# Kernel optimization log

Measured on AMD Instinct MI355X. Metric: run time of the kernel, lower is better.

The kernel has to match this reference:

```python
import jax, jax.numpy as jnp
import numpy as np

T, B, NIN, N, A = 100, 32, 512, 2048, 2
DT = 1e-3
THR = 1.0
ALPHA = float(np.exp(-DT / 0.01))


def setup_inputs() -> dict:
    key = jax.random.key(0)
    k1, k2, k3, k4 = jax.random.split(key, 4)
    rates = jax.random.uniform(k1, (T, B, NIN), dtype=jnp.float32) * 100.0  # Hz
    noise = jax.random.uniform(k2, (T, B, NIN), dtype=jnp.float32)  # Poisson thresholds
    Win = jax.random.normal(k3, (A, NIN, N), dtype=jnp.float32) * (1.5 / np.sqrt(NIN))
    Wrec = jax.random.normal(k4, (A, A, N, N), dtype=jnp.float32) * (1.0 / np.sqrt(N))
    return {"rates": rates, "noise": noise, "Win": Win, "Wrec": Wrec}


def reference(rates, noise, Win, Wrec):
    dtype = rates.dtype
    V0 = jnp.zeros((A, B, N), dtype)   # membrane potentials, all areas
    Xd0 = jnp.zeros((A, B, N), dtype)  # delayed cross-area spikes (reset())

    def step(carry, inp):
        V, Xd = carry
        rate_t, noise_t = inp
        # PoissonInput: Bernoulli spikes with prob rate*dt
        Xi = (noise_t < rate_t * DT).astype(dtype)  # [B, NIN]
        # per-area input current: feedforward + all-to-all cross-area recurrent
        I = jnp.einsum('bi,ain->abn', Xi, Win) + jnp.einsum('sbn,sanm->abm', Xd, Wrec)
        # LIF: leak, reset on previous spike, integrate
        V_new = ALPHA * V * (1.0 - Xd) + I
        S = (V_new >= THR).astype(dtype)  # [A, B, N]
        return (V_new, S), (Xi, S)

    (_, _), (Xis, Ss) = jax.lax.scan(step, (V0, Xd0), (rates, noise))
    # Xis: [T, B, NIN]; Ss: [T, A, B, N] -> per-area stacked outputs
    return (Xis, Ss[:, 0], Ss[:, 1])
```

## Files before the change

kernel.cpp:

```cpp
#include <hip/hip_runtime.h>

#define T_STEPS 100
#define BATCH   32
#define NIN     512
#define NN      2048
#define AREAS   2

#define ALPHA_D 0.9048374180359595

__global__ __launch_bounds__(256)
void k0_xi(const float* __restrict__ rates, const float* __restrict__ noise,
           float* __restrict__ outXi, unsigned* __restrict__ xi_mask)
{
    int el = blockIdx.x * 256 + threadIdx.x;
    float r = rates[el], nz = noise[el];
    float p = __fmul_rn(r, 0.001f);
    int spike = (nz < p) ? 1 : 0;
    outXi[el] = (float)spike;
    if (spike) {
        int t = el >> 14;
        int b = (el >> 9) & 31;
        int i = el & (NIN - 1);
        atomicOr(&xi_mask[(t * 32 + b) * 16 + (i >> 5)], 1u << (i & 31));
    }
}

__global__ __launch_bounds__(256)
void k_ff(const float* __restrict__ Win, const unsigned* __restrict__ xi_mask,
          float* __restrict__ Iff)
{
    const int tb  = blockIdx.x;
    const int a   = blockIdx.y;
    const int tid = threadIdx.x;

    __shared__ unsigned mws[16];
    if (tid < 16) mws[tid] = xi_mask[tb * 16 + tid];
    __syncthreads();

    const float* Wa = Win + ((size_t)a << 20) + (tid << 3);
    float4 A0 = {0,0,0,0}, A1 = {0,0,0,0};
    for (int w = 0; w < 16; ++w) {
        unsigned mw = mws[w];
        int base_i = w << 5;
        while (mw) {
            int i = base_i + (__ffs(mw) - 1);
            mw &= mw - 1;
            const float* rp = Wa + ((size_t)i << 11);
            float4 w0 = ((const float4*)rp)[0];
            float4 w1 = ((const float4*)rp)[1];
            A0.x += w0.x; A0.y += w0.y; A0.z += w0.z; A0.w += w0.w;
            A1.x += w1.x; A1.y += w1.y; A1.z += w1.z; A1.w += w1.w;
        }
    }
    float* op = Iff + (((size_t)tb * 2 + a) << 11) + (tid << 3);
    ((float4*)op)[0] = A0;
    ((float4*)op)[1] = A1;
}

#define OFF_OF(rr) ((((rr) >> 11) << 23) + (((rr) & 2047) << 11))

__device__ __forceinline__ void issue8(const float* __restrict__ Wa,
                                       const unsigned short* lp, float* p)
{
    uint4 u = *(const uint4*)lp;
    p[0] = Wa[OFF_OF((int)(u.x & 0xffff))];
    p[1] = Wa[OFF_OF((int)(u.x >> 16))];
    p[2] = Wa[OFF_OF((int)(u.y & 0xffff))];
    p[3] = Wa[OFF_OF((int)(u.y >> 16))];
    p[4] = Wa[OFF_OF((int)(u.z & 0xffff))];
    p[5] = Wa[OFF_OF((int)(u.z >> 16))];
    p[6] = Wa[OFF_OF((int)(u.w & 0xffff))];
    p[7] = Wa[OFF_OF((int)(u.w >> 16))];
}

__global__ __launch_bounds__(256, 2)
void k_steps(const float* __restrict__ Wrec,
             unsigned long long* __restrict__ smask,
             const float* __restrict__ Iff,
             float* __restrict__ outS)
{
    const int tid = threadIdx.x;
    const int bx  = blockIdx.x;
    const int s   = bx & 15;
    const int b   = bx >> 4;
    const int a   = s >> 3;
    const int m0  = (s & 7) << 8;
    const int c   = m0 + tid;

    __shared__ unsigned mws[128];
    __shared__ __align__(16) unsigned short lrec[AREAS * NN];
    __shared__ int base[128];
    __shared__ int cnt_rec;
    __shared__ unsigned nsp[8];

    const float* __restrict__ Wa = Wrec + ((size_t)a << 22) + c;
    const int rr_self = (a << 11) | c;
    const int wsel = rr_self >> 5;
    const int w0   = s << 3;

    float vst = 0.0f;

    for (int t = 0; t < T_STEPS; ++t) {
        unsigned long long* cur = smask + (size_t)(t & 1) * (BATCH * 128) + (b << 7);
        unsigned long long* nxt = smask + (size_t)((t + 1) & 1) * (BATCH * 128) + (b << 7);

        if (tid < 128) {
            unsigned long long v = __hip_atomic_load(&cur[tid], __ATOMIC_RELAXED,
                                                     __HIP_MEMORY_SCOPE_AGENT);
            while ((unsigned)(v >> 32) != (unsigned)t) {
                __builtin_amdgcn_s_sleep(4);
                v = __hip_atomic_load(&cur[tid], __ATOMIC_RELAXED,
                                      __HIP_MEMORY_SCOPE_AGENT);
            }
            mws[tid] = (unsigned)v;
        }
        if (tid < 8) nsp[tid] = 0u;
        float accf = Iff[((((size_t)t * BATCH + b) * 2 + a) << 11) + c];
        __syncthreads();

        if (tid < 64) {
            int c0 = __popc(mws[2 * tid]), c1 = __popc(mws[2 * tid + 1]);
            int cc = c0 + c1, incl = cc;
            #pragma unroll
            for (int d = 1; d < 64; d <<= 1) {
                int v = __shfl_up(incl, d, 64);
                if (tid >= d) incl += v;
            }
            base[2 * tid]     = incl - cc;
            base[2 * tid + 1] = incl - c1;
            if (tid == 63) cnt_rec = incl;
        }
        __syncthreads();

        if (tid < 128) {
            unsigned w = mws[tid];
            if (w) {
                int off = base[tid];
                int bb = tid << 5;
                while (w) {
                    int p = __ffs(w) - 1;
                    lrec[off++] = (unsigned short)(bb + p);
                    w &= w - 1;
                }
            }
        }
        __syncthreads();

        const int nrec = cnt_rec;
        unsigned xd = (mws[wsel] >> (tid & 31)) & 1u;

        float accr = 0.0f;
        int j = 0;
        if (nrec >= 32) {
            float p[32], q[32];
            issue8(Wa, &lrec[0],  p + 0);
            issue8(Wa, &lrec[8],  p + 8);
            issue8(Wa, &lrec[16], p + 16);
            issue8(Wa, &lrec[24], p + 24);
            for (j = 32; j + 32 <= nrec; j += 32) {
                issue8(Wa, &lrec[j],      q + 0);
                issue8(Wa, &lrec[j + 8],  q + 8);
                issue8(Wa, &lrec[j + 16], q + 16);
                issue8(Wa, &lrec[j + 24], q + 24);
                #pragma unroll
                for (int k = 0; k < 32; ++k) accr = __fadd_rn(accr, p[k]);
                #pragma unroll
                for (int k = 0; k < 32; ++k) p[k] = q[k];
            }
            #pragma unroll
            for (int k = 0; k < 32; ++k) accr = __fadd_rn(accr, p[k]);
        }
        if (nrec - j >= 8) {
            float p[8], q[8];
            issue8(Wa, &lrec[j], p);
            int jj = j + 8;
            for (; jj + 8 <= nrec; jj += 8) {
                issue8(Wa, &lrec[jj], q);
                #pragma unroll
                for (int k = 0; k < 8; ++k) accr = __fadd_rn(accr, p[k]);
                #pragma unroll
                for (int k = 0; k < 8; ++k) p[k] = q[k];
            }
            #pragma unroll
            for (int k = 0; k < 8; ++k) accr = __fadd_rn(accr, p[k]);
            j = jj;
        }
        for (; j < nrec; ++j) {
            int rr = lrec[j];
            accr = __fadd_rn(accr, Wa[OFF_OF(rr)]);
        }

        float I  = __fadd_rn(accf, accr);
        float v  = __fmul_rn((float)ALPHA_D, vst);
        if (xd) v = 0.0f;
        float vn = __fadd_rn(v, I);
        vst = vn;
        int S = (vn >= 1.0f) ? 1 : 0;
        if (S) atomicOr(&nsp[tid >> 5], 1u << (tid & 31));
        __syncthreads();

        if (t < T_STEPS - 1 && tid < 8) {
            unsigned long long pv =
                ((unsigned long long)(unsigned)(t + 1) << 32) | nsp[tid];
            atomicExch(&nxt[w0 + tid], pv);
        }
        outS[(size_t)a * (T_STEPS * BATCH * NN)
             + (((size_t)t * BATCH + b) << 11) + c] = (float)S;
    }
}
#undef OFF_OF

extern "C" void kernel_launch(void* const* d_in, const int* in_sizes, int n_in,
                              void* d_out, int out_size, void* d_ws, size_t ws_size,
                              hipStream_t stream)
{
    const float* rates = (const float*)d_in[0];
    const float* noise = (const float*)d_in[1];
    const float* Win   = (const float*)d_in[2];
    const float* Wrec  = (const float*)d_in[3];
    float* out = (float*)d_out;

    char* ws = (char*)d_ws;
    unsigned* xi_mask = (unsigned*)ws;
    unsigned long long* smask = (unsigned long long*)(ws + 204800);
    float* Iff = (float*)(ws + 270336);

    hipMemsetAsync(d_ws, 0, 270336, stream);

    k0_xi<<<6400, 256, 0, stream>>>(rates, noise, out, xi_mask);
    k_ff<<<dim3(3200, 2), 256, 0, stream>>>(Win, xi_mask, Iff);

    float* outS = out + (size_t)T_STEPS * BATCH * NIN;
    void* args[] = { (void*)&Wrec, (void*)&smask, (void*)&Iff, (void*)&outS };
    hipLaunchCooperativeKernel((const void*)k_steps, dim3(512), dim3(256),
                               args, 0, stream);
}
```

Measured before the change: 1.221 ms.

## Stage recurrent weight rows into LDS via global_load_lds dwordx4

```diff
diff --git a/kernel.cpp b/kernel.cpp
--- a/kernel.cpp
+++ b/kernel.cpp
@@ -59,19 +59,9 @@
 
 #define OFF_OF(rr) ((((rr) >> 11) << 23) + (((rr) & 2047) << 11))
 
-__device__ __forceinline__ void issue8(const float* __restrict__ Wa,
-                                       const unsigned short* lp, float* p)
-{
-    uint4 u = *(const uint4*)lp;
-    p[0] = Wa[OFF_OF((int)(u.x & 0xffff))];
-    p[1] = Wa[OFF_OF((int)(u.x >> 16))];
-    p[2] = Wa[OFF_OF((int)(u.y & 0xffff))];
-    p[3] = Wa[OFF_OF((int)(u.y >> 16))];
-    p[4] = Wa[OFF_OF((int)(u.z & 0xffff))];
-    p[5] = Wa[OFF_OF((int)(u.z >> 16))];
-    p[6] = Wa[OFF_OF((int)(u.w & 0xffff))];
-    p[7] = Wa[OFF_OF((int)(u.w >> 16))];
-}
+#define GLDS(src, dst) __builtin_amdgcn_global_load_lds(                      \
+    (const __attribute__((address_space(1))) void*)(src),                     \
+    (__attribute__((address_space(3))) void*)(dst), 16, 0, 0)
 
 __global__ __launch_bounds__(256, 2)
 void k_steps(const float* __restrict__ Wrec,
@@ -86,14 +76,17 @@
     const int a   = s >> 3;
     const int m0  = (s & 7) << 8;
     const int c   = m0 + tid;
-
+    const int wv  = tid >> 6;
+    const int lane = tid & 63;
+
+    __shared__ __align__(16) float stage[64 * 256];
     __shared__ unsigned mws[128];
     __shared__ __align__(16) unsigned short lrec[AREAS * NN];
     __shared__ int base[128];
     __shared__ int cnt_rec;
     __shared__ unsigned nsp[8];
 
-    const float* __restrict__ Wa = Wrec + ((size_t)a << 22) + c;
+    const float* __restrict__ Wb = Wrec + ((size_t)a << 22) + m0 + (lane << 2);
     const int rr_self = (a << 11) | c;
     const int wsel = rr_self >> 5;
     const int w0   = s << 3;
@@ -150,44 +143,29 @@
         unsigned xd = (mws[wsel] >> (tid & 31)) & 1u;
 
         float accr = 0.0f;
-        int j = 0;
-        if (nrec >= 32) {
-            float p[32], q[32];
-            issue8(Wa, &lrec[0],  p + 0);
-            issue8(Wa, &lrec[8],  p + 8);
-            issue8(Wa, &lrec[16], p + 16);
-            issue8(Wa, &lrec[24], p + 24);
-            for (j = 32; j + 32 <= nrec; j += 32) {
-                issue8(Wa, &lrec[j],      q + 0);
-                issue8(Wa, &lrec[j + 8],  q + 8);
-                issue8(Wa, &lrec[j + 16], q + 16);
-                issue8(Wa, &lrec[j + 24], q + 24);
-                #pragma unroll
-                for (int k = 0; k < 32; ++k) accr = __fadd_rn(accr, p[k]);
-                #pragma unroll
-                for (int k = 0; k < 32; ++k) p[k] = q[k];
-            }
-            #pragma unroll
-            for (int k = 0; k < 32; ++k) accr = __fadd_rn(accr, p[k]);
-        }
-        if (nrec - j >= 8) {
-            float p[8], q[8];
-            issue8(Wa, &lrec[j], p);
-            int jj = j + 8;
-            for (; jj + 8 <= nrec; jj += 8) {
-                issue8(Wa, &lrec[jj], q);
-                #pragma unroll
-                for (int k = 0; k < 8; ++k) accr = __fadd_rn(accr, p[k]);
-                #pragma unroll
-                for (int k = 0; k < 8; ++k) p[k] = q[k];
-            }
-            #pragma unroll
-            for (int k = 0; k < 8; ++k) accr = __fadd_rn(accr, p[k]);
-            j = jj;
-        }
-        for (; j < nrec; ++j) {
-            int rr = lrec[j];
-            accr = __fadd_rn(accr, Wa[OFF_OF(rr)]);
+        for (int j = 0; j < nrec; j += 64) {
+            const int cnt = min(64, nrec - j);
+            for (int k = wv; k < cnt; k += 4) {
+                int row = lrec[j + k];
+                GLDS(Wb + OFF_OF(row), &stage[k << 8]);
+            }
+            asm volatile("s_waitcnt vmcnt(0)" ::: "memory");
+            __builtin_amdgcn_sched_barrier(0);
+            __syncthreads();
+            int k = 0;
+            for (; k + 4 <= cnt; k += 4) {
+                float w0v = stage[((k + 0) << 8) + tid];
+                float w1v = stage[((k + 1) << 8) + tid];
+                float w2v = stage[((k + 2) << 8) + tid];
+                float w3v = stage[((k + 3) << 8) + tid];
+                accr = __fadd_rn(accr, w0v);
+                accr = __fadd_rn(accr, w1v);
+                accr = __fadd_rn(accr, w2v);
+                accr = __fadd_rn(accr, w3v);
+            }
+            for (; k < cnt; ++k)
+                accr = __fadd_rn(accr, stage[(k << 8) + tid]);
+            __syncthreads();
         }
 
         float I  = __fadd_rn(accf, accr);
@@ -209,6 +187,7 @@
     }
 }
 #undef OFF_OF
+#undef GLDS
 
 extern "C" void kernel_launch(void* const* d_in, const int* in_sizes, int n_in,
                               void* d_out, int out_size, void* d_ws, size_t ws_size,
```

Result: faster. 1.090 ms (-10.7%).
